# Kernel optimization log

Hardware: AMD Instinct MI355X
Metric: run time of the kernel (lower is better)

The kernel has to match this reference:

```python
import jax, jax.numpy as jnp
import numpy as np

B, F, H, K, E = 512, 1280, 2560, 8, 9  # batch, feat_dim, 2*feat_dim, branching, n_internal
# Tree: root=node 0 (expert 0); level-1 nodes 1..8 (experts 1..8); level-2 leaves 9..72.

def setup_inputs() -> dict:
    key = jax.random.key(0)
    k0, k1, k2, k3, k4 = jax.random.split(key, 5)
    x = jax.random.normal(k0, (B, F), dtype=jnp.float32)
    W1 = jax.random.normal(k1, (E, F, H), dtype=jnp.float32) / np.sqrt(F)
    b1 = jnp.zeros((E, H), dtype=jnp.float32)
    W2 = jax.random.normal(k2, (E, H, K), dtype=jnp.float32) / np.sqrt(H)
    b2 = jnp.zeros((E, K), dtype=jnp.float32)
    return {"x": x, "W1": W1, "b1": b1, "W2": W2, "b2": b2}

def reference(x, W1, b1, W2, b2):
    # Batched experts: Linear(F->H) -> ReLU -> Linear(H->K), softmax over children.
    h = jax.nn.relu(jnp.einsum('bf,efh->ebh', x, W1) + b1[:, None, :])  # [E,B,H]
    logits = jnp.einsum('ebh,ehk->ebk', h, W2) + b2[:, None, :]          # [E,B,K]
    probs = jax.nn.softmax(logits, axis=-1)                              # [E,B,K]
    # Path products root->node for every node (matches leaf_probs in torch code).
    p0 = jnp.ones((1, x.shape[0]), dtype=x.dtype)        # root: prob 1        [1,B]
    p1 = probs[0].T                                       # nodes 1..8          [K,B]
    # leaves 9..72: parent of node n is 1+(n-9)//K, child index (n-9)%K
    p2 = (p1[:, None, :] * jnp.transpose(probs[1:E], (0, 2, 1))).reshape(K * K, -1)  # [64,B]
    leaf_probs = jnp.concatenate([p0, p1, p2], axis=0).T  # [B, 73]
    return leaf_probs, logits
```

## Files before the change

kernel.cpp:

```cpp
#include <hip/hip_runtime.h>

#define TB 512
#define TF 1280
#define TH 2560
#define TK 8
#define TE 9

typedef unsigned short ushortT;
typedef unsigned long long u64;
typedef __attribute__((ext_vector_type(8))) short short8;
typedef __attribute__((ext_vector_type(4))) short short4v;
typedef __attribute__((ext_vector_type(4))) float floatx4;

__device__ __forceinline__ unsigned short f2bf(float f) {
  union { float f; unsigned u; } v; v.f = f;
  unsigned r = v.u + 0x7fffu + ((v.u >> 16) & 1u);
  return (unsigned short)(r >> 16);
}

__device__ __forceinline__ unsigned pk2(float a, float b) {
  union { float f; unsigned u; } ua, ub; ua.f = a; ub.f = b;
  unsigned ra = ua.u + 0x7fffu + ((ua.u >> 16) & 1u);
  unsigned rb = ub.u + 0x7fffu + ((ub.u >> 16) & 1u);
  return __builtin_amdgcn_perm(rb, ra, 0x07060302);
}

__device__ __forceinline__ void gl_lds16(const void* g, void* l) {
  __builtin_amdgcn_global_load_lds(
      (const __attribute__((address_space(1))) unsigned*)g,
      (__attribute__((address_space(3))) unsigned*)l, 16, 0, 0);
}

__global__ __launch_bounds__(256) void prepass(
    const float* __restrict__ x, const float* __restrict__ W2,
    u64* __restrict__ xq, ushortT* __restrict__ W2t) {
  const int i = blockIdx.x * 256 + threadIdx.x;
  if (i < 320 * 512) {
    const int kq = i >> 9, m = i & 511;
    floatx4 v = *(const floatx4*)(x + (long)m * TF + kq * 4);
    xq[i] = (u64)pk2(v.x, v.y) | ((u64)pk2(v.z, v.w) << 32);
  } else {
    const int o = i - 320 * 512;
    if (o < TE * TK * TH) {
      const int hcol = o % TH;
      const int rest = o / TH;
      const int n = rest & 7;
      const int e = rest >> 3;
      W2t[(long)(e * TK + n) * TH + hcol] = f2bf(W2[((long)e * TH + hcol) * TK + n]);
    }
  }
}

__global__ __launch_bounds__(256) void pack_w1(const float* __restrict__ W1,
                                               u64* __restrict__ W1p) {
  const int bid = blockIdx.x;
  const int nt = bid % 10;
  const int kt = (bid / 10) % 80;
  const int e  = bid / 800;
  const int t = threadIdx.x;
  const int tk = t >> 6, tc = t & 63;
  const int k0 = kt * 16 + tk * 4;
  const int n0 = nt * 256 + tc * 4;
  const float* src = W1 + ((long)e * TF + k0) * TH + n0;
  floatx4 v0 = *(const floatx4*)(src);
  floatx4 v1 = *(const floatx4*)(src + TH);
  floatx4 v2 = *(const floatx4*)(src + 2 * TH);
  floatx4 v3 = *(const floatx4*)(src + 3 * TH);
  u64 q[4];
#pragma unroll
  for (int i = 0; i < 4; ++i)
    q[i] = (u64)pk2(v0[i], v1[i]) | ((u64)pk2(v2[i], v3[i]) << 32);
  u64* dst = W1p + ((long)(e * 320 + (k0 >> 2)) * TH + n0);
  *(ulonglong2*)(dst)     = make_ulonglong2(q[0], q[1]);
  *(ulonglong2*)(dst + 2) = make_ulonglong2(q[2], q[3]);
}

__global__ __launch_bounds__(256) void gemm1_relu(
    const u64* __restrict__ xq, const u64* __restrict__ W1p,
    const float* __restrict__ b1, ushortT* __restrict__ h) {
  __shared__ __align__(16) u64 Aq[8 * 132];
  __shared__ __align__(16) u64 Bq[8 * 132];
  const int t = threadIdx.x;
  const int lane = t & 63, w = t >> 6;
  const int bid = blockIdx.x;
  const int mt = bid & 3;
  const int ctile = bid >> 2;
  const int e = ctile / 20;
  const int hbase = (ctile % 20) * 128;
  const int m0 = mt * 128;
  const int wm = w & 1, wn = w >> 1;
  const int lm = lane & 15, lq = lane >> 4;

  const u64* agB = xq + m0 + lane * 2;
  const u64* bgB = W1p + ((long)e * 320) * TH + hbase + lane * 2;

  floatx4 acc[4][4];
#pragma unroll
  for (int i = 0; i < 4; ++i)
#pragma unroll
    for (int j = 0; j < 4; ++j) acc[i][j] = (floatx4){0.f, 0.f, 0.f, 0.f};

  for (int kt = 0; kt < 40; ++kt) {
    const int r0 = kt * 8;
    gl_lds16(agB + (long)(r0 + w) * 512, &Aq[w * 132]);
    gl_lds16(agB + (long)(r0 + w + 4) * 512, &Aq[(w + 4) * 132]);
    gl_lds16(bgB + (long)(r0 + w) * TH, &Bq[w * 132]);
    gl_lds16(bgB + (long)(r0 + w + 4) * TH, &Bq[(w + 4) * 132]);
    __syncthreads();

    short8 af[4], bf[4];
#pragma unroll
    for (int mg = 0; mg < 4; ++mg) {
      const int m = wm * 64 + mg * 16 + lm;
      ((u64*)&af[mg])[0] = Aq[(2 * lq) * 132 + m];
      ((u64*)&af[mg])[1] = Aq[(2 * lq + 1) * 132 + m];
    }
#pragma unroll
    for (int ng = 0; ng < 4; ++ng) {
      const int n = wn * 64 + ng * 16 + lm;
      ((u64*)&bf[ng])[0] = Bq[(2 * lq) * 132 + n];
      ((u64*)&bf[ng])[1] = Bq[(2 * lq + 1) * 132 + n];
    }
#pragma unroll
    for (int mg = 0; mg < 4; ++mg)
#pragma unroll
      for (int ng = 0; ng < 4; ++ng)
        acc[mg][ng] = __builtin_amdgcn_mfma_f32_16x16x32_bf16(af[mg], bf[ng], acc[mg][ng], 0, 0, 0);
    __syncthreads();
  }

#pragma unroll
  for (int mg = 0; mg < 4; ++mg) {
    const int row = m0 + wm * 64 + mg * 16 + lq * 4;
#pragma unroll
    for (int ng = 0; ng < 4; ++ng) {
      const int col = hbase + wn * 64 + ng * 16 + lm;
      const float bias = b1[e * TH + col];
      floatx4 c = acc[mg][ng];
#pragma unroll
      for (int r = 0; r < 4; ++r) {
        float v = c[r] + bias;
        v = v > 0.f ? v : 0.f;
        h[((long)e * TB + row + r) * TH + col] = f2bf(v);
      }
    }
  }
}

__global__ __launch_bounds__(256) void gemm1_fb(
    const float* __restrict__ x, const float* __restrict__ W1,
    const float* __restrict__ b1, ushortT* __restrict__ h) {
  __shared__ __align__(16) ushortT As[128 * 40];
  __shared__ __align__(16) ushortT Bs[128 * 40];
  const int t = threadIdx.x;
  const int tileN = blockIdx.x;
  const int e = tileN / 20;
  const int hbase = (tileN % 20) * 128;
  const int m0 = blockIdx.y * 128;
  const int lane = t & 63, w = t >> 6;
  const int wm = w & 1, wn = w >> 1;
  const int lm = lane & 15, lq = lane >> 4;
  const int lk = lq * 8;
  floatx4 acc[4][4];
#pragma unroll
  for (int i = 0; i < 4; ++i)
#pragma unroll
    for (int j = 0; j < 4; ++j) acc[i][j] = (floatx4){0.f, 0.f, 0.f, 0.f};
  const float* wp = W1 + (long)e * TF * TH + hbase;
  const int cA = (t & 7) * 4;
  const int mA = t >> 3;
  const int nB = t & 127;
  const int gB = t >> 7;
  for (int kt = 0; kt < TF / 32; ++kt) {
    const int k0 = kt * 32;
    if (kt) __syncthreads();
#pragma unroll
    for (int i = 0; i < 4; ++i) {
      const int m = mA + 32 * i;
      floatx4 v = *(const floatx4*)(x + (long)(m0 + m) * TF + k0 + cA);
      short4v s; s.x = f2bf(v.x); s.y = f2bf(v.y); s.z = f2bf(v.z); s.w = f2bf(v.w);
      *(short4v*)&As[m * 40 + cA] = s;
    }
    {
      const float* bp = wp + (long)k0 * TH + nB;
#pragma unroll
      for (int q = 0; q < 4; ++q) {
        const int k4 = gB * 16 + q * 4;
        float f0 = bp[(long)(k4 + 0) * TH];
        float f1 = bp[(long)(k4 + 1) * TH];
        float f2 = bp[(long)(k4 + 2) * TH];
        float f3 = bp[(long)(k4 + 3) * TH];
        short4v s; s.x = f2bf(f0); s.y = f2bf(f1); s.z = f2bf(f2); s.w = f2bf(f3);
        *(short4v*)&Bs[nB * 40 + k4] = s;
      }
    }
    __syncthreads();
    short8 af[4], bfr[4];
#pragma unroll
    for (int mg = 0; mg < 4; ++mg)
      af[mg] = *(const short8*)&As[(wm * 64 + mg * 16 + lm) * 40 + lk];
#pragma unroll
    for (int ng = 0; ng < 4; ++ng)
      bfr[ng] = *(const short8*)&Bs[(wn * 64 + ng * 16 + lm) * 40 + lk];
#pragma unroll
    for (int mg = 0; mg < 4; ++mg)
#pragma unroll
      for (int ng = 0; ng < 4; ++ng)
        acc[mg][ng] = __builtin_amdgcn_mfma_f32_16x16x32_bf16(af[mg], bfr[ng], acc[mg][ng], 0, 0, 0);
  }
#pragma unroll
  for (int mg = 0; mg < 4; ++mg) {
    const int row = m0 + wm * 64 + mg * 16 + lq * 4;
#pragma unroll
    for (int ng = 0; ng < 4; ++ng) {
      const int col = hbase + wn * 64 + ng * 16 + lm;
      const float bias = b1[e * TH + col];
      floatx4 c = acc[mg][ng];
#pragma unroll
      for (int r = 0; r < 4; ++r) {
        float v = c[r] + bias;
        v = v > 0.f ? v : 0.f;
        h[((long)e * TB + row + r) * TH + col] = f2bf(v);
      }
    }
  }
}

__global__ __launch_bounds__(256) void gemm2_softmax(
    const ushortT* __restrict__ h, const ushortT* __restrict__ W2t,
    const float* __restrict__ b2, float* __restrict__ logits_out,
    float* __restrict__ probs) {
  __shared__ float Ls[4][16][8];
  const int t = threadIdx.x;
  const int lane = t & 63, w = t >> 6;
  const int e = blockIdx.x >> 5;
  const int r0 = (blockIdx.x & 31) * 16;
  const int lm = lane & 15, lq = lane >> 4;

  const ushortT* hp = h + ((long)(e * TB + r0 + lm)) * TH + w * 640 + lq * 8;
  const int bn = lm < 8 ? lm : 7;
  const ushortT* wp = W2t + ((long)(e * TK + bn)) * TH + w * 640 + lq * 8;

  floatx4 acc = (floatx4){0.f, 0.f, 0.f, 0.f};
#pragma unroll
  for (int kt = 0; kt < 20; ++kt) {
    short8 a = *(const short8*)(hp + kt * 32);
    short8 b = *(const short8*)(wp + kt * 32);
    acc = __builtin_amdgcn_mfma_f32_16x16x32_bf16(a, b, acc, 0, 0, 0);
  }
  if (lm < 8) {
#pragma unroll
    for (int r = 0; r < 4; ++r) Ls[w][lq * 4 + r][lm] = acc[r];
  }
  __syncthreads();
  if (w == 0 && lm < 8) {
    const float bias = b2[e * TK + lm];
#pragma unroll
    for (int r = 0; r < 4; ++r) {
      const int row = lq * 4 + r;
      float v = Ls[0][row][lm] + Ls[1][row][lm] + Ls[2][row][lm] + Ls[3][row][lm] + bias;
      float mx = v;
      mx = fmaxf(mx, __shfl_xor(mx, 1, 64));
      mx = fmaxf(mx, __shfl_xor(mx, 2, 64));
      mx = fmaxf(mx, __shfl_xor(mx, 4, 64));
      float ex = __expf(v - mx);
      float sm = ex;
      sm += __shfl_xor(sm, 1, 64);
      sm += __shfl_xor(sm, 2, 64);
      sm += __shfl_xor(sm, 4, 64);
      const long idx = ((long)e * TB + r0 + row) * TK + lm;
      logits_out[idx] = v;
      probs[idx] = ex / sm;
    }
  }
}

__global__ __launch_bounds__(256) void leafk(const float* __restrict__ probs,
                                             float* __restrict__ out) {
  const int idx = blockIdx.x * 256 + threadIdx.x;
  if (idx >= TB * 73) return;
  const int b = idx / 73, c = idx % 73;
  float v;
  if (c == 0) {
    v = 1.0f;
  } else if (c < 9) {
    v = probs[(long)b * TK + (c - 1)];
  } else {
    const int i = (c - 9) >> 3, j = (c - 9) & 7;
    v = probs[(long)b * TK + i] * probs[((long)(1 + i) * TB + b) * TK + j];
  }
  out[idx] = v;
}

extern "C" void kernel_launch(void* const* d_in, const int* in_sizes, int n_in,
                              void* d_out, int out_size, void* d_ws, size_t ws_size,
                              hipStream_t stream) {
  const float* x  = (const float*)d_in[0];
  const float* W1 = (const float*)d_in[1];
  const float* b1 = (const float*)d_in[2];
  const float* W2 = (const float*)d_in[3];
  const float* b2 = (const float*)d_in[4];
  float* out = (float*)d_out;

  ushortT* h     = (ushortT*)d_ws;
  float*   probs = (float*)((char*)d_ws + 23592960);
  u64*     xq    = (u64*)((char*)d_ws + 23740416);
  ushortT* W2t   = (ushortT*)((char*)d_ws + 25051136);
  u64*     W1p   = (u64*)((char*)d_ws + 25419776);
  const size_t NEED = 25419776 + 58982400;
  float* logits_out = out + TB * 73;

  if (ws_size >= NEED) {
    prepass<<<1360, 256, 0, stream>>>(x, W2, xq, W2t);
    pack_w1<<<7200, 256, 0, stream>>>(W1, W1p);
    gemm1_relu<<<720, 256, 0, stream>>>(xq, W1p, b1, h);
  } else {
    prepass<<<1360, 256, 0, stream>>>(x, W2, xq, W2t);
    gemm1_fb<<<dim3(180, 4), 256, 0, stream>>>(x, W1, b1, h);
  }
  gemm2_softmax<<<TE * 32, 256, 0, stream>>>(h, W2t, b2, logits_out, probs);
  leafk<<<(TB * 73 + 255) / 256, 256, 0, stream>>>(probs, out);
}
```

Measured before the change: 241.9 us.

## Merge prep kernels, swizzle gemm1 blocks per XCD, widen gemm2 K-split

The W1 packing, x quantisation and W2 transpose now run in a single prep kernel, removing one launch and letting the two pieces of work share the GPU. gemm1 block indices are remapped so that blocks landing on the same XCD get consecutive tiles and can reuse W1p data in that XCD's L2. gemm2_softmax runs with 8 waves instead of 4, each handling half as much K, giving more parallelism at the cost of a larger LDS reduction.

```diff
diff --git a/kernel.cpp b/kernel.cpp
--- a/kernel.cpp
+++ b/kernel.cpp
@@ -29,6 +29,50 @@
   __builtin_amdgcn_global_load_lds(
       (const __attribute__((address_space(1))) unsigned*)g,
       (__attribute__((address_space(3))) unsigned*)l, 16, 0, 0);
+}
+
+__global__ __launch_bounds__(256) void prep_all(
+    const float* __restrict__ x, const float* __restrict__ W1,
+    const float* __restrict__ W2,
+    u64* __restrict__ xq, ushortT* __restrict__ W2t, u64* __restrict__ W1p) {
+  const int b = blockIdx.x;
+  const int t = threadIdx.x;
+  if (b < 7200) {
+    const int nt = b % 10;
+    const int kt = (b / 10) % 80;
+    const int e  = b / 800;
+    const int tk = t >> 6, tc = t & 63;
+    const int k0 = kt * 16 + tk * 4;
+    const int n0 = nt * 256 + tc * 4;
+    const float* src = W1 + ((long)e * TF + k0) * TH + n0;
+    floatx4 v0 = *(const floatx4*)(src);
+    floatx4 v1 = *(const floatx4*)(src + TH);
+    floatx4 v2 = *(const floatx4*)(src + 2 * TH);
+    floatx4 v3 = *(const floatx4*)(src + 3 * TH);
+    u64 q[4];
+#pragma unroll
+    for (int i = 0; i < 4; ++i)
+      q[i] = (u64)pk2(v0[i], v1[i]) | ((u64)pk2(v2[i], v3[i]) << 32);
+    u64* dst = W1p + ((long)(e * 320 + (k0 >> 2)) * TH + n0);
+    *(ulonglong2*)(dst)     = make_ulonglong2(q[0], q[1]);
+    *(ulonglong2*)(dst + 2) = make_ulonglong2(q[2], q[3]);
+  } else {
+    const int i = (b - 7200) * 256 + t;
+    if (i < 320 * 512) {
+      const int kq = i >> 9, m = i & 511;
+      floatx4 v = *(const floatx4*)(x + (long)m * TF + kq * 4);
+      xq[i] = (u64)pk2(v.x, v.y) | ((u64)pk2(v.z, v.w) << 32);
+    } else {
+      const int o = i - 320 * 512;
+      if (o < TE * TK * TH) {
+        const int hcol = o % TH;
+        const int rest = o / TH;
+        const int n = rest & 7;
+        const int e = rest >> 3;
+        W2t[(long)(e * TK + n) * TH + hcol] = f2bf(W2[((long)e * TH + hcol) * TK + n]);
+      }
+    }
+  }
 }
 
 __global__ __launch_bounds__(256) void prepass(
@@ -51,30 +95,6 @@
   }
 }
 
-__global__ __launch_bounds__(256) void pack_w1(const float* __restrict__ W1,
-                                               u64* __restrict__ W1p) {
-  const int bid = blockIdx.x;
-  const int nt = bid % 10;
-  const int kt = (bid / 10) % 80;
-  const int e  = bid / 800;
-  const int t = threadIdx.x;
-  const int tk = t >> 6, tc = t & 63;
-  const int k0 = kt * 16 + tk * 4;
-  const int n0 = nt * 256 + tc * 4;
-  const float* src = W1 + ((long)e * TF + k0) * TH + n0;
-  floatx4 v0 = *(const floatx4*)(src);
-  floatx4 v1 = *(const floatx4*)(src + TH);
-  floatx4 v2 = *(const floatx4*)(src + 2 * TH);
-  floatx4 v3 = *(const floatx4*)(src + 3 * TH);
-  u64 q[4];
-#pragma unroll
-  for (int i = 0; i < 4; ++i)
-    q[i] = (u64)pk2(v0[i], v1[i]) | ((u64)pk2(v2[i], v3[i]) << 32);
-  u64* dst = W1p + ((long)(e * 320 + (k0 >> 2)) * TH + n0);
-  *(ulonglong2*)(dst)     = make_ulonglong2(q[0], q[1]);
-  *(ulonglong2*)(dst + 2) = make_ulonglong2(q[2], q[3]);
-}
-
 __global__ __launch_bounds__(256) void gemm1_relu(
     const u64* __restrict__ xq, const u64* __restrict__ W1p,
     const float* __restrict__ b1, ushortT* __restrict__ h) {
@@ -82,7 +102,8 @@
   __shared__ __align__(16) u64 Bq[8 * 132];
   const int t = threadIdx.x;
   const int lane = t & 63, w = t >> 6;
-  const int bid = blockIdx.x;
+  const int bid0 = blockIdx.x;
+  const int bid = (bid0 & 7) * 90 + (bid0 >> 3);
   const int mt = bid & 3;
   const int ctile = bid >> 2;
   const int e = ctile / 20;
@@ -226,24 +247,24 @@
   }
 }
 
-__global__ __launch_bounds__(256) void gemm2_softmax(
+__global__ __launch_bounds__(512) void gemm2_softmax(
     const ushortT* __restrict__ h, const ushortT* __restrict__ W2t,
     const float* __restrict__ b2, float* __restrict__ logits_out,
     float* __restrict__ probs) {
-  __shared__ float Ls[4][16][8];
+  __shared__ float Ls[8][16][8];
   const int t = threadIdx.x;
   const int lane = t & 63, w = t >> 6;
   const int e = blockIdx.x >> 5;
   const int r0 = (blockIdx.x & 31) * 16;
   const int lm = lane & 15, lq = lane >> 4;
 
-  const ushortT* hp = h + ((long)(e * TB + r0 + lm)) * TH + w * 640 + lq * 8;
+  const ushortT* hp = h + ((long)(e * TB + r0 + lm)) * TH + w * 320 + lq * 8;
   const int bn = lm < 8 ? lm : 7;
-  const ushortT* wp = W2t + ((long)(e * TK + bn)) * TH + w * 640 + lq * 8;
+  const ushortT* wp = W2t + ((long)(e * TK + bn)) * TH + w * 320 + lq * 8;
 
   floatx4 acc = (floatx4){0.f, 0.f, 0.f, 0.f};
 #pragma unroll
-  for (int kt = 0; kt < 20; ++kt) {
+  for (int kt = 0; kt < 10; ++kt) {
     short8 a = *(const short8*)(hp + kt * 32);
     short8 b = *(const short8*)(wp + kt * 32);
     acc = __builtin_amdgcn_mfma_f32_16x16x32_bf16(a, b, acc, 0, 0, 0);
@@ -258,7 +279,9 @@
 #pragma unroll
     for (int r = 0; r < 4; ++r) {
       const int row = lq * 4 + r;
-      float v = Ls[0][row][lm] + Ls[1][row][lm] + Ls[2][row][lm] + Ls[3][row][lm] + bias;
+      float v = Ls[0][row][lm] + Ls[1][row][lm] + Ls[2][row][lm] + Ls[3][row][lm]
+              + Ls[4][row][lm] + Ls[5][row][lm] + Ls[6][row][lm] + Ls[7][row][lm]
+              + bias;
       float mx = v;
       mx = fmaxf(mx, __shfl_xor(mx, 1, 64));
       mx = fmaxf(mx, __shfl_xor(mx, 2, 64));
@@ -311,13 +334,12 @@
   float* logits_out = out + TB * 73;
 
   if (ws_size >= NEED) {
-    prepass<<<1360, 256, 0, stream>>>(x, W2, xq, W2t);
-    pack_w1<<<7200, 256, 0, stream>>>(W1, W1p);
+    prep_all<<<8560, 256, 0, stream>>>(x, W1, W2, xq, W2t, W1p);
     gemm1_relu<<<720, 256, 0, stream>>>(xq, W1p, b1, h);
   } else {
     prepass<<<1360, 256, 0, stream>>>(x, W2, xq, W2t);
     gemm1_fb<<<dim3(180, 4), 256, 0, stream>>>(x, W1, b1, h);
   }
-  gemm2_softmax<<<TE * 32, 256, 0, stream>>>(h, W2t, b2, logits_out, probs);
+  gemm2_softmax<<<TE * 32, 512, 0, stream>>>(h, W2t, b2, logits_out, probs);
   leafk<<<(TB * 73 + 255) / 256, 256, 0, stream>>>(probs, out);
 }
```

Result: faster. 232.1 us (-4.0%).
